# Kernel optimization log

Measured on AMD Instinct MI355X. Metric: run time of the kernel, lower is better.

## Reference

```python
import jax, jax.numpy as jnp
import numpy as np

B, N, C, H, K = 2, 4096, 256, 8, 32
D = C // H
EPS = 1e-5


def _ln(x, w, b):
    # LayerNorm over last axis
    m = x.mean(-1, keepdims=True)
    v = x.var(-1, keepdims=True)
    return (x - m) * jax.lax.rsqrt(v + EPS) * w + b


def setup_inputs() -> dict:
    key = jax.random.key(0)
    ks = jax.random.split(key, 16)
    s = 1.0 / np.sqrt(C)
    inp = {
        'xyz_A': jax.random.normal(ks[0], (B, N, 3), jnp.float32),
        'xyz_B': jax.random.normal(ks[1], (B, N, 3), jnp.float32),
        'featA': jax.random.normal(ks[2], (B, C, N), jnp.float32),
        'featB': jax.random.normal(ks[3], (B, C, N), jnp.float32),
        'ln_in_w': jnp.ones((C,), jnp.float32), 'ln_in_b': jnp.zeros((C,), jnp.float32),
        'wq': jax.random.normal(ks[4], (C, C), jnp.float32) * s, 'bq': jnp.zeros((C,), jnp.float32),
        'wk': jax.random.normal(ks[5], (C, C), jnp.float32) * s, 'bk': jnp.zeros((C,), jnp.float32),
        'wv': jax.random.normal(ks[6], (C, C), jnp.float32) * s, 'bv': jnp.zeros((C,), jnp.float32),
        'wqd': jax.random.normal(ks[7], (C, C), jnp.float32) * s, 'bqd': jnp.zeros((C,), jnp.float32),
        'wkd': jax.random.normal(ks[8], (C, C), jnp.float32) * s, 'bkd': jnp.zeros((C,), jnp.float32),
        'ln_sim_w': jnp.ones((C,), jnp.float32), 'ln_sim_b': jnp.zeros((C,), jnp.float32),
        'ln_dis_w': jnp.ones((C,), jnp.float32), 'ln_dis_b': jnp.zeros((C,), jnp.float32),
        'fus_w1': jax.random.normal(ks[9], (2 * C, 3 * C), jnp.float32) * (1.0 / np.sqrt(3 * C)),
        'bn_g': jnp.ones((2 * C,), jnp.float32), 'bn_b': jnp.zeros((2 * C,), jnp.float32),
        'fus_w2': jax.random.normal(ks[10], (C, 2 * C), jnp.float32) * (1.0 / np.sqrt(2 * C)),
        'fus_b2': jnp.zeros((C,), jnp.float32),
    }
    return inp


def reference(xyz_A, xyz_B, featA, featB, ln_in_w, ln_in_b,
              wq, bq, wk, bk, wv, bv, wqd, bqd, wkd, bkd,
              ln_sim_w, ln_sim_b, ln_dis_w, ln_dis_b,
              fus_w1, bn_g, bn_b, fus_w2, fus_b2):
    xA = featA.transpose(0, 2, 1)   # (B,N,C)
    xB = featB.transpose(0, 2, 1)   # (B,N,C)
    xA_n = _ln(xA, ln_in_w, ln_in_b)

    # KNN: nearest K points of xyz_B for each point in xyz_A
    d2 = (jnp.sum(xyz_A * xyz_A, -1)[:, :, None]
          + jnp.sum(xyz_B * xyz_B, -1)[:, None, :]
          - 2.0 * jnp.einsum('bnc,bmc->bnm', xyz_A, xyz_B))  # (B,N,N)
    _, knn_idx = jax.lax.top_k(-d2, K)  # (B,N,K)

    def proj(x, W, b):  # Conv1d k=1 on (B,N,C)
        return jnp.einsum('bnc,oc->bno', x, W) + b

    def heads(x):
        return x.reshape(B, N, H, D)

    q_s = heads(proj(xA_n, wq, bq))
    k_s = heads(proj(xB, wk, bk))
    v = heads(proj(xB, wv, bv))

    gather = jax.vmap(lambda f, i: f[i])  # (N,H,D),(N,K) -> (N,K,H,D)
    kN = gather(k_s, knn_idx)   # (B,N,K,H,D)
    vN = gather(v, knn_idx)     # (B,N,K,H,D)

    # similarity path: scaled dot-product over K neighbors
    sim = jnp.einsum('bnhd,bnkhd->bnhk', q_s, kN) / jnp.sqrt(jnp.float32(D))
    w_sim = jax.nn.softmax(sim, -1)
    ctx_s = jnp.einsum('bnhk,bnkhd->bnhd', w_sim, vN).reshape(B, N, C)
    ctx_s = _ln(ctx_s, ln_sim_w, ln_sim_b)

    # dissimilarity path: L2 distance scores
    q_d = heads(proj(xA_n, wqd, bqd))
    k_d = heads(proj(xB, wkd, bkd))
    kdN = gather(k_d, knn_idx)  # (B,N,K,H,D)
    diff = q_d[:, :, None] - kdN
    dist = jnp.sqrt(jnp.sum(diff * diff, -1)).transpose(0, 1, 3, 2)  # (B,N,H,K)
    w_dis = jax.nn.softmax(dist, -1)
    ctx_d = jnp.einsum('bnhk,bnkhd->bnhd', w_dis, vN).reshape(B, N, C)
    ctx_d = _ln(ctx_d, ln_dis_w, ln_dis_b)

    # fusion MLP (BN in eval mode: running mean 0, var 1)
    fused = jnp.concatenate([xA_n, ctx_s, ctx_d], -1)  # (B,N,3C)
    y = jnp.einsum('bnc,oc->bno', fused, fus_w1)
    y = y * jax.lax.rsqrt(jnp.float32(1.0 + EPS)) * bn_g + bn_b
    y = jax.nn.relu(y)
    y = jnp.einsum('bnc,oc->bno', y, fus_w2) + fus_b2

    out = y + xA  # residual (identity since in_channel == out_channel)
    return out.transpose(0, 2, 1)  # (B,C,N)
```

## Files before the change

kernel.cpp:

```cpp
#include <hip/hip_runtime.h>
#include <hip/hip_bf16.h>
#include <math.h>

#define B_ 2
#define N_ 4096
#define C_ 256
#define H_ 8
#define K_ 32
#define NP_ (B_*N_)
#define CAPW 256

typedef __attribute__((ext_vector_type(8))) short bf16x8;
typedef __attribute__((ext_vector_type(4))) float f32x4;

__device__ __forceinline__ float bf2f(unsigned short v){
    union { unsigned int u; float f; } x; x.u = ((unsigned int)v) << 16; return x.f;
}
__device__ __forceinline__ unsigned short f2bf(float f){
    union { float f; unsigned int u; } x; x.f = f;
    return (unsigned short)((x.u + 0x7FFFu + ((x.u >> 16) & 1u)) >> 16);
}
__device__ __forceinline__ unsigned int mono(float f){
    union { float f; unsigned int u; } x; x.f = f;
    return x.u ^ (0x80000000u | (unsigned int)((int)x.u >> 31));
}
__device__ __forceinline__ void gload_lds16(const unsigned short* g, unsigned short* l){
    __builtin_amdgcn_global_load_lds(
        (const __attribute__((address_space(1))) unsigned int*)g,
        (__attribute__((address_space(3))) unsigned int*)l, 16, 0, 0);
}

__global__ __launch_bounds__(256) void k_pre(
    const float* __restrict__ s0, const float* __restrict__ s1,
    const float* __restrict__ s2, const float* __restrict__ s3,
    const float* __restrict__ s4, const float* __restrict__ s5,
    const float* __restrict__ s6, unsigned short* __restrict__ Wb,
    const float* __restrict__ xyzB, f32x4* __restrict__ PB,
    const float* __restrict__ xyzA, int* __restrict__ order,
    const float* __restrict__ featA, const float* __restrict__ lnw,
    const float* __restrict__ lnb, unsigned short* __restrict__ F,
    const float* __restrict__ featB, unsigned short* __restrict__ XBT)
{
    __shared__ __align__(16) char smem[35200];
    const int bid = blockIdx.x;
    const int tid = threadIdx.x;
    if (bid < 3328){
        int i = bid*256 + tid;
        float v;
        if (i < 327680){
            int seg = i >> 16, off = i & 65535;
            const float* s = (seg==0)?s0:(seg==1)?s1:(seg==2)?s2:(seg==3)?s3:s4;
            v = s[off];
        } else if (i < 720896){
            v = s5[i - 327680];
        } else {
            v = s6[i - 720896];
        }
        Wb[i] = f2bf(v);
    } else if (bid < 3360){
        int i = (bid - 3328)*256 + tid;
        float x = xyzB[i*3], y = xyzB[i*3+1], z = xyzB[i*3+2];
        f32x4 o;
        o[0] = -2.f*x; o[1] = -2.f*y; o[2] = -2.f*z;
        o[3] = x*x + y*y + z*z;
        PB[i] = o;
    } else if (bid < 3362){
        unsigned int* hist = (unsigned int*)smem;
        unsigned int* wsum = (unsigned int*)(smem + 4096);
        const int b = bid - 3360;
        const int wv = tid >> 6, lane = tid & 63;
        for (int i = tid; i < 1024; i += 256) hist[i] = 0u;
        __syncthreads();
        unsigned int code[16];
        #pragma unroll
        for (int i = 0; i < 16; i++){
            const int n = tid + i*256;
            const float* pp = xyzA + (size_t)((b<<12) + n)*3;
            int qx = (int)fminf(fmaxf((pp[0] + 5.f)*1.6f, 0.f), 15.f);
            int qy = (int)fminf(fmaxf((pp[1] + 5.f)*0.8f, 0.f), 7.f);
            int qz = (int)fminf(fmaxf((pp[2] + 5.f)*0.8f, 0.f), 7.f);
            unsigned int c = (unsigned int)((qx & 1) | ((qz & 1) << 1) | ((qy & 1) << 2)
                           | (((qx >> 1) & 1) << 3) | (((qz >> 1) & 1) << 4) | (((qy >> 1) & 1) << 5)
                           | (((qx >> 2) & 1) << 6) | (((qz >> 2) & 1) << 7) | (((qy >> 2) & 1) << 8)
                           | (((qx >> 3) & 1) << 9));
            code[i] = c;
            atomicAdd(&hist[c], 1u);
        }
        __syncthreads();
        unsigned int loc[4], t4 = 0;
        #pragma unroll
        for (int j = 0; j < 4; j++){ loc[j] = hist[tid*4 + j]; t4 += loc[j]; }
        unsigned int sc = t4;
        #pragma unroll
        for (int off = 1; off < 64; off <<= 1){
            unsigned int o = __shfl_up(sc, off, 64);
            if (lane >= off) sc += o;
        }
        if (lane == 63) wsum[wv] = sc;
        __syncthreads();
        unsigned int wb = 0;
        #pragma unroll
        for (int j = 0; j < 4; j++) if (j < wv) wb += wsum[j];
        unsigned int base = wb + sc - t4;
        #pragma unroll
        for (int j = 0; j < 4; j++){ hist[tid*4 + j] = base; base += loc[j]; }
        __syncthreads();
        #pragma unroll
        for (int i = 0; i < 16; i++){
            const int n = tid + i*256;
            unsigned int pos = atomicAdd(&hist[code[i]], 1u);
            order[(b<<12) + pos] = (b<<12) | n;
        }
    } else if (bid < 3618){
        float (*tile)[257] = (float(*)[257])smem;
        float (*ps)[32]    = (float(*)[32])(smem + 32896);
        float (*pq)[32]    = (float(*)[32])(smem + 33920);
        float (*st)[32]    = (float(*)[32])(smem + 34944);
        const int nx = tid & 31, cy = tid >> 5;
        const int pbase = (bid - 3362) * 32;
        const int b = pbase >> 12, n0 = pbase & 4095;
        const float* sp = featA + (size_t)b*C_*N_ + n0;
        #pragma unroll 4
        for (int it = 0; it < 32; it++){
            int c = cy + it*8;
            tile[nx][c] = sp[(size_t)c*N_ + nx];
        }
        __syncthreads();
        {
            float s = 0.f, q = 0.f;
            #pragma unroll 8
            for (int i = 0; i < 32; i++){
                int cc = cy*32 + ((i + cy) & 31);
                float x = tile[nx][cc];
                s += x; q = fmaf(x, x, q);
            }
            ps[cy][nx] = s; pq[cy][nx] = q;
        }
        __syncthreads();
        if (tid < 32){
            float S = 0.f, Q = 0.f;
            #pragma unroll
            for (int j = 0; j < 8; j++){ S += ps[j][tid]; Q += pq[j][tid]; }
            float m = S*(1.f/256.f);
            float v = Q*(1.f/256.f) - m*m;
            st[0][tid] = m; st[1][tid] = rsqrtf(v + 1e-5f);
        }
        __syncthreads();
        const int p = pbase + nx;
        const float m = st[0][nx], r = st[1][nx];
        #pragma unroll
        for (int j = 0; j < 4; j++){
            bf16x8 ob;
            #pragma unroll
            for (int e = 0; e < 8; e++){
                int c = cy*32 + j*8 + e;
                ob[e] = (short)f2bf((tile[nx][c]-m)*r*lnw[c] + lnb[c]);
            }
            *(bf16x8*)(F + (size_t)p*768 + cy*32 + j*8) = ob;
        }
    } else {
        float (*tile)[65] = (float(*)[65])smem;
        const int idx = bid - 3618;
        const int x = idx & 63, y = (idx >> 6) & 3, z = idx >> 8;
        const int n0 = x*64, c0 = y*64;
        const int tx = tid & 63, ty = tid >> 6;
        const float* sp = featB + (size_t)z*C_*N_;
        #pragma unroll
        for (int i = 0; i < 16; i++){
            int cr = ty + i*4;
            tile[cr][tx] = sp[(size_t)(c0+cr)*N_ + n0 + tx];
        }
        __syncthreads();
        const int c = c0 + tx;
        #pragma unroll
        for (int i = 0; i < 16; i++){
            int nr = ty + i*4;
            int p = (z<<12) + n0 + nr;
            XBT[(size_t)p*256 + c] = f2bf(tile[tx][nr]);
        }
    }
}

__global__ __launch_bounds__(256) void k_knn(const float* __restrict__ xyzA,
        const f32x4* __restrict__ PB, int* __restrict__ knn){
    const int wv = threadIdx.x >> 6, lane = threadIdx.x & 63;
    const int p = blockIdx.x*4 + wv;
    const int b = p >> 12;
    const f32x4* pb = PB + ((size_t)b << 12);
    const float ax = xyzA[(size_t)p*3], ay = xyzA[(size_t)p*3+1], az = xyzA[(size_t)p*3+2];

    unsigned long long mn = ~0ull;
    #pragma unroll 8
    for (int i = 0; i < 64; i++){
        const int m = i*64 + lane;
        f32x4 c = pb[m];
        float d = fmaf(ax, c[0], fmaf(ay, c[1], fmaf(az, c[2], c[3])));
        unsigned long long key = (((unsigned long long)mono(d)) << 12) | (unsigned int)m;
        mn = key < mn ? key : mn;
    }
    unsigned int rk = 0;
    for (int j = 0; j < 64; j++){
        unsigned long long o = __shfl(mn, j, 64);
        rk += (o < mn) ? 1u : 0u;
    }
    unsigned long long sel = (rk == 31u) ? mn : ~0ull;
    #pragma unroll
    for (int off = 32; off; off >>= 1){
        unsigned long long o = __shfl_xor(sel, off, 64);
        sel = o < sel ? o : sel;
    }
    const unsigned long long v = sel;
    const unsigned int vhi = (unsigned int)(v >> 12);
    const unsigned int vlo = (unsigned int)(v & 0xFFFull);

    __shared__ unsigned long long cand[4][CAPW];
    __shared__ unsigned int cnt[4];
    if (lane == 0) cnt[wv] = 0u;
    #pragma unroll 8
    for (int i = 0; i < 64; i++){
        const int m = i*64 + lane;
        f32x4 c = pb[m];
        float d = fmaf(ax, c[0], fmaf(ay, c[1], fmaf(az, c[2], c[3])));
        unsigned int u = mono(d);
        if (u < vhi || (u == vhi && (unsigned int)m <= vlo)){
            unsigned int slot = atomicAdd(&cnt[wv], 1u);
            if (slot < CAPW)
                cand[wv][slot] = (((unsigned long long)u) << 12) | (unsigned int)m;
        }
    }
    const unsigned int C = cnt[wv];
    if (C <= CAPW){
        for (unsigned int i = lane; i < C; i += 64){
            unsigned long long mk = cand[wv][i];
            unsigned int rank = 0;
            for (unsigned int j = 0; j < C; j++) rank += (cand[wv][j] < mk) ? 1u : 0u;
            if (rank < K_) knn[(size_t)p*K_ + rank] = (int)(mk & 0xFFFull);
        }
    } else {
        unsigned long long last = 0ull;
        for (int it = 0; it < K_; it++){
            unsigned long long cm = ~0ull;
            #pragma unroll 4
            for (int i = 0; i < 64; i++){
                const int m = i*64 + lane;
                f32x4 c = pb[m];
                float d = fmaf(ax, c[0], fmaf(ay, c[1], fmaf(az, c[2], c[3])));
                unsigned long long key = (((unsigned long long)mono(d)) << 12) | (unsigned int)m;
                if (key > last && key < cm) cm = key;
            }
            #pragma unroll
            for (int off = 32; off; off >>= 1){
                unsigned long long o = __shfl_xor(cm, off, 64);
                cm = o < cm ? o : cm;
            }
            if (lane == 0) knn[(size_t)p*K_ + it] = (int)(cm & 0xFFFull);
            last = cm;
        }
    }
}

template<int MODE>
__device__ __forceinline__ void gemm_body(
    const unsigned short* __restrict__ X, int ldx,
    const unsigned short* __restrict__ W, int Kin,
    const float* __restrict__ e0, const float* __restrict__ e1, const float* __restrict__ e2,
    unsigned short* __restrict__ Y, int ldy,
    const float* __restrict__ resid, float* __restrict__ out,
    unsigned short (*As)[128*32], unsigned short (*Bs)[64*32], int bx, int by)
{
    const int tid = threadIdx.x, wid = tid >> 6, lane = tid & 63;
    const int lr = lane & 15, lg = lane >> 4;
    const int m0 = bx*128, n0 = by*64;
    const int lrow = lane >> 2, lcol = (lane & 3)*8;

    const unsigned short* Ag0 = X + (size_t)(m0 + wid*32 + lrow)*ldx + lcol;
    const unsigned short* Ag1 = X + (size_t)(m0 + wid*32 + 16 + lrow)*ldx + lcol;
    const unsigned short* Bg0 = W + (size_t)(n0 + wid*16 + lrow)*Kin + lcol;

    f32x4 acc[2][4] = {};
    const int NT = Kin >> 5;
    int buf = 0;
    gload_lds16(Ag0, &As[0][(wid*32)*32]);
    gload_lds16(Ag1, &As[0][(wid*32+16)*32]);
    gload_lds16(Bg0, &Bs[0][(wid*16)*32]);
    __syncthreads();
    for (int kt = 0; kt < NT; kt++){
        if (kt + 1 < NT){
            const int k = (kt+1)*32;
            gload_lds16(Ag0 + k, &As[buf^1][(wid*32)*32]);
            gload_lds16(Ag1 + k, &As[buf^1][(wid*32+16)*32]);
            gload_lds16(Bg0 + k, &Bs[buf^1][(wid*16)*32]);
        }
        bf16x8 a[2], b[4];
        #pragma unroll
        for (int mi = 0; mi < 2; mi++)
            a[mi] = *(const bf16x8*)&As[buf][(wid*32 + mi*16 + lr)*32 + lg*8];
        #pragma unroll
        for (int ni = 0; ni < 4; ni++)
            b[ni] = *(const bf16x8*)&Bs[buf][(ni*16 + lr)*32 + lg*8];
        #pragma unroll
        for (int mi = 0; mi < 2; mi++){
            #pragma unroll
            for (int ni = 0; ni < 4; ni++)
                acc[mi][ni] = __builtin_amdgcn_mfma_f32_16x16x32_bf16(a[mi], b[ni], acc[mi][ni], 0, 0, 0);
        }
        __syncthreads();
        buf ^= 1;
    }
    #pragma unroll
    for (int mi = 0; mi < 2; mi++){
        const int pbase = m0 + wid*32 + mi*16 + lg*4;
        #pragma unroll
        for (int ni = 0; ni < 4; ni++){
            const int o = n0 + ni*16 + lr;
            if (MODE == 0){
                const float* bp = (o < 256) ? e0 : ((o < 512) ? e1 : e2);
                float bias = bp[o & 255];
                #pragma unroll
                for (int r = 0; r < 4; r++)
                    Y[(size_t)(pbase + r)*ldy + o] = f2bf(acc[mi][ni][r] + bias);
            } else if (MODE == 1){
                float sc = e0[o] * 0.9999950000374997f;
                float sh = e1[o];
                #pragma unroll
                for (int r = 0; r < 4; r++){
                    float vv = fmaf(acc[mi][ni][r], sc, sh);
                    Y[(size_t)(pbase + r)*ldy + o] = f2bf(fmaxf(vv, 0.f));
                }
            } else {
                float bias = e0[o];
                const int b = pbase >> 12, nn = pbase & 4095;
                const size_t adr = ((size_t)b*C_ + o)*N_ + nn;
                f32x4 rv = *(const f32x4*)(resid + adr);
                f32x4 ov;
                #pragma unroll
                for (int r = 0; r < 4; r++) ov[r] = acc[mi][ni][r] + bias + rv[r];
                *(f32x4*)(out + adr) = ov;
            }
        }
    }
}

__global__ __launch_bounds__(256) void k_proj(
    const unsigned short* __restrict__ F, const unsigned short* __restrict__ XBT,
    const unsigned short* __restrict__ WQcat, const unsigned short* __restrict__ WKVD,
    const float* __restrict__ bq, const float* __restrict__ bqd,
    const float* __restrict__ bk, const float* __restrict__ bv, const float* __restrict__ bkd,
    unsigned short* __restrict__ QQ, unsigned short* __restrict__ KVD)
{
    __shared__ __align__(16) unsigned short As[2][128*32];
    __shared__ __align__(16) unsigned short Bs[2][64*32];
    if (blockIdx.y < 8)
        gemm_body<0>(F, 768, WQcat, 256, bq, bqd, nullptr, QQ, 512, nullptr, nullptr,
                     As, Bs, blockIdx.x, blockIdx.y);
    else
        gemm_body<0>(XBT, 256, WKVD, 256, bk, bv, bkd, KVD, 768, nullptr, nullptr,
                     As, Bs, blockIdx.x, blockIdx.y - 8);
}

template<int MODE>
__global__ __launch_bounds__(256) void k_gemm(
    const unsigned short* __restrict__ X, int ldx,
    const unsigned short* __restrict__ W, int Kin,
    const float* __restrict__ e0, const float* __restrict__ e1, const float* __restrict__ e2,
    unsigned short* __restrict__ Y, int ldy,
    const float* __restrict__ resid, float* __restrict__ out)
{
    __shared__ __align__(16) unsigned short As[2][128*32];
    __shared__ __align__(16) unsigned short Bs[2][64*32];
    gemm_body<MODE>(X, ldx, W, Kin, e0, e1, e2, Y, ldy, resid, out,
                    As, Bs, blockIdx.x, blockIdx.y);
}

__global__ __launch_bounds__(256) void k_attn(
    const unsigned short* __restrict__ QQ, const unsigned short* __restrict__ KVD,
    const int* __restrict__ KNN, const int* __restrict__ order,
    const float* __restrict__ lnsw, const float* __restrict__ lnsb,
    const float* __restrict__ lndw, const float* __restrict__ lndb,
    unsigned short* __restrict__ F)
{
    __shared__ float q_l[2][2][2][128];
    __shared__ float w_l[2][2][2][4][33];
    __shared__ int   idx_l[2][2][32];
    __shared__ float part_l[2][2][4];

    const int tid = threadIdx.x;
    const int wid = tid >> 6, lane = tid & 63;
    const int ps = wid >> 1, wh = wid & 1;
    const int bid = blockIdx.x;
    const int xcd = bid & 7, ib = bid >> 3;
    const int batch = xcd & 1, quarter = xcd >> 1;
    const int jj = quarter*1024 + ib*2 + ps;
    const int p = order[(batch << 12) + jj];
    const int b = batch;

    {
        const unsigned short* qrow = QQ + (size_t)p*512 + wh*128 + lane*2;
        unsigned int us = *(const unsigned int*)qrow;
        unsigned int ud = *(const unsigned int*)(qrow + 256);
        q_l[ps][wh][0][lane*2]   = bf2f((unsigned short)(us & 0xffff));
        q_l[ps][wh][0][lane*2+1] = bf2f((unsigned short)(us >> 16));
        q_l[ps][wh][1][lane*2]   = bf2f((unsigned short)(ud & 0xffff));
        q_l[ps][wh][1][lane*2+1] = bf2f((unsigned short)(ud >> 16));
        if (lane < 32) idx_l[ps][wh][lane] = KNN[(size_t)p*K_ + lane];
    }

    const int hh = lane >> 5, kk = lane & 31;
    const int tq = lane >> 4, c = lane & 15;
    const int hl = c >> 2;

    const int nbr_qk = idx_l[ps][wh][kk];
    int nbt[8];
    #pragma unroll
    for (int i = 0; i < 8; i++) nbt[i] = idx_l[ps][wh][tq + i*4];

    const unsigned short* rowb = KVD + (size_t)((b<<12) + nbr_qk)*768;
    bf16x8 kx[2][4], dx[2][4];
    #pragma unroll
    for (int j = 0; j < 2; j++){
        const int h = wh*4 + j*2 + hh;
        const bf16x8* kr = (const bf16x8*)(rowb + h*32);
        const bf16x8* dr = (const bf16x8*)(rowb + 512 + h*32);
        #pragma unroll
        for (int cc = 0; cc < 4; cc++){ kx[j][cc] = kr[cc]; dx[j][cc] = dr[cc]; }
    }
    const unsigned short* vbase = KVD + 256 + wh*128 + c*8;
    bf16x8 vx[8];
    #pragma unroll
    for (int i = 0; i < 8; i++)
        vx[i] = *(const bf16x8*)(vbase + (size_t)((b<<12) + nbt[i])*768);

    #pragma unroll
    for (int j = 0; j < 2; j++){
        const int hloc = j*2 + hh;
        const float* qs = &q_l[ps][wh][0][hloc*32];
        const float* qd = &q_l[ps][wh][1][hloc*32];
        float s = 0.f, dd = 0.f;
        #pragma unroll
        for (int cc = 0; cc < 4; cc++){
            #pragma unroll
            for (int e = 0; e < 8; e++){
                const int d = cc*8 + e;
                s = fmaf(qs[d], bf2f((unsigned short)kx[j][cc][e]), s);
                float df = qd[d] - bf2f((unsigned short)dx[j][cc][e]);
                dd = fmaf(df, df, dd);
            }
        }
        float sim = s * 0.17677669529663687f;
        float dist = sqrtf(dd);
        float m1 = sim, m2 = dist;
        #pragma unroll
        for (int off = 1; off < 32; off <<= 1){
            m1 = fmaxf(m1, __shfl_xor(m1, off, 64));
            m2 = fmaxf(m2, __shfl_xor(m2, off, 64));
        }
        float e1v = __expf(sim - m1);
        float e2v = __expf(dist - m2);
        float s1 = e1v, s2 = e2v;
        #pragma unroll
        for (int off = 1; off < 32; off <<= 1){
            s1 += __shfl_xor(s1, off, 64);
            s2 += __shfl_xor(s2, off, 64);
        }
        w_l[ps][wh][0][hloc][kk] = e1v / s1;
        w_l[ps][wh][1][hloc][kk] = e2v / s2;
    }

    float cs[8] = {0,0,0,0,0,0,0,0}, cd[8] = {0,0,0,0,0,0,0,0};
    #pragma unroll
    for (int i = 0; i < 8; i++){
        const int t = tq + i*4;
        const float wsv = w_l[ps][wh][0][hl][t];
        const float wdv = w_l[ps][wh][1][hl][t];
        #pragma unroll
        for (int e = 0; e < 8; e++){
            float vf = bf2f((unsigned short)vx[i][e]);
            cs[e] = fmaf(wsv, vf, cs[e]);
            cd[e] = fmaf(wdv, vf, cd[e]);
        }
    }
    #pragma unroll
    for (int e = 0; e < 8; e++){
        cs[e] += __shfl_xor(cs[e], 16, 64); cs[e] += __shfl_xor(cs[e], 32, 64);
        cd[e] += __shfl_xor(cd[e], 16, 64); cd[e] += __shfl_xor(cd[e], 32, 64);
    }
    float s1 = 0.f, q1 = 0.f, s2 = 0.f, q2 = 0.f;
    #pragma unroll
    for (int e = 0; e < 8; e++){
        s1 += cs[e]; q1 = fmaf(cs[e], cs[e], q1);
        s2 += cd[e]; q2 = fmaf(cd[e], cd[e], q2);
    }
    #pragma unroll
    for (int off = 1; off < 16; off <<= 1){
        s1 += __shfl_xor(s1, off, 64); q1 += __shfl_xor(q1, off, 64);
        s2 += __shfl_xor(s2, off, 64); q2 += __shfl_xor(q2, off, 64);
    }
    if (lane == 0){
        part_l[ps][wh][0] = s1; part_l[ps][wh][1] = q1;
        part_l[ps][wh][2] = s2; part_l[ps][wh][3] = q2;
    }
    __syncthreads();
    const float S1 = s1 + part_l[ps][wh^1][0];
    const float Q1 = q1 + part_l[ps][wh^1][1];
    const float S2 = s2 + part_l[ps][wh^1][2];
    const float Q2 = q2 + part_l[ps][wh^1][3];
    const float m1 = S1*(1.f/256.f), m2 = S2*(1.f/256.f);
    const float r1 = rsqrtf(Q1*(1.f/256.f) - m1*m1 + 1e-5f);
    const float r2 = rsqrtf(Q2*(1.f/256.f) - m2*m2 + 1e-5f);

    if (tq == 0){
        bf16x8 ob;
        #pragma unroll
        for (int e = 0; e < 8; e++){
            const int cg = wh*128 + c*8 + e;
            ob[e] = (short)f2bf((cs[e]-m1)*r1*lnsw[cg] + lnsb[cg]);
        }
        *(bf16x8*)(F + (size_t)p*768 + 256 + wh*128 + c*8) = ob;
    } else if (tq == 1){
        bf16x8 ob;
        #pragma unroll
        for (int e = 0; e < 8; e++){
            const int cg = wh*128 + c*8 + e;
            ob[e] = (short)f2bf((cd[e]-m2)*r2*lndw[cg] + lndb[cg]);
        }
        *(bf16x8*)(F + (size_t)p*768 + 512 + wh*128 + c*8) = ob;
    }
}

extern "C" void kernel_launch(void* const* d_in, const int* in_sizes, int n_in,
                              void* d_out, int out_size, void* d_ws, size_t ws_size,
                              hipStream_t stream)
{
    const float* xyzA   = (const float*)d_in[0];
    const float* xyzB   = (const float*)d_in[1];
    const float* featA  = (const float*)d_in[2];
    const float* featB  = (const float*)d_in[3];
    const float* ln_in_w= (const float*)d_in[4];
    const float* ln_in_b= (const float*)d_in[5];
    const float* wq  = (const float*)d_in[6];
    const float* bq  = (const float*)d_in[7];
    const float* wk  = (const float*)d_in[8];
    const float* bk  = (const float*)d_in[9];
    const float* wv  = (const float*)d_in[10];
    const float* bv  = (const float*)d_in[11];
    const float* wqd = (const float*)d_in[12];
    const float* bqd = (const float*)d_in[13];
    const float* wkd = (const float*)d_in[14];
    const float* bkd = (const float*)d_in[15];
    const float* lnsw = (const float*)d_in[16];
    const float* lnsb = (const float*)d_in[17];
    const float* lndw = (const float*)d_in[18];
    const float* lndb = (const float*)d_in[19];
    const float* fw1 = (const float*)d_in[20];
    const float* bng = (const float*)d_in[21];
    const float* bnb = (const float*)d_in[22];
    const float* fw2 = (const float*)d_in[23];
    const float* fb2 = (const float*)d_in[24];
    float* out = (float*)d_out;
    char* ws = (char*)d_ws;

    unsigned short* F    = (unsigned short*)(ws + 0);
    unsigned short* XBT  = (unsigned short*)(ws + 12582912);
    unsigned short* QQ   = (unsigned short*)(ws + 16777216);
    unsigned short* KVD  = (unsigned short*)(ws + 25165824);
    unsigned short* Y1   = (unsigned short*)(ws + 37748736);
    f32x4*          PB   = (f32x4*)(ws + 37748736);
    int*            KNNi = (int*)(ws + 46137344);
    int*            ORD  = (int*)(ws + 47185920);
    unsigned short* Wb   = (unsigned short*)(ws + 47251456);
    unsigned short* WQcat = Wb;
    unsigned short* WKVD  = Wb + 131072;
    unsigned short* W1b   = Wb + 327680;
    unsigned short* W2b   = Wb + 720896;

    k_pre<<<4130, 256, 0, stream>>>(wq, wqd, wk, wv, wkd, fw1, fw2, Wb,
                                    xyzB, PB, xyzA, ORD,
                                    featA, ln_in_w, ln_in_b, F, featB, XBT);
    k_knn<<<2048, 256, 0, stream>>>(xyzA, PB, KNNi);

    k_proj<<<dim3(64,20), 256, 0, stream>>>(F, XBT, WQcat, WKVD, bq, bqd, bk, bv, bkd, QQ, KVD);

    k_attn<<<4096, 256, 0, stream>>>(QQ, KVD, KNNi, ORD, lnsw, lnsb, lndw, lndb, F);

    k_gemm<1><<<dim3(64,8), 256, 0, stream>>>(F,  768, W1b, 768, bng, bnb, nullptr, Y1, 512, nullptr, nullptr);
    k_gemm<2><<<dim3(64,4), 256, 0, stream>>>(Y1, 512, W2b, 512, fb2, nullptr, nullptr, nullptr, 0, featA, out);
}
```

Before: 142.0 us.

## Process two query points per wave in attention and vectorize weight conversion

The attention kernel now has each wave handle two query points instead of one, interleaving their K/D/V gathers, dot products, softmaxes and LayerNorm reductions. This halves the grid and raises memory-level parallelism and ILP per wave. The weight-conversion section of the preprocessing kernel now converts four floats per thread with vector loads and stores, cutting that section's block count by a factor of four. The cost is higher register pressure in the attention kernel, which could lower occupancy.

```diff
diff --git a/kernel.cpp b/kernel.cpp
--- a/kernel.cpp
+++ b/kernel.cpp
@@ -12,6 +12,7 @@
 
 typedef __attribute__((ext_vector_type(8))) short bf16x8;
 typedef __attribute__((ext_vector_type(4))) float f32x4;
+typedef __attribute__((ext_vector_type(4))) unsigned short ushort4_t;
 
 __device__ __forceinline__ float bf2f(unsigned short v){
     union { unsigned int u; float f; } x; x.u = ((unsigned int)v) << 16; return x.f;
@@ -44,30 +45,34 @@
     __shared__ __align__(16) char smem[35200];
     const int bid = blockIdx.x;
     const int tid = threadIdx.x;
-    if (bid < 3328){
-        int i = bid*256 + tid;
-        float v;
+    if (bid < 832){
+        int i = (bid*256 + tid)*4;
+        const float* s; int off;
         if (i < 327680){
-            int seg = i >> 16, off = i & 65535;
-            const float* s = (seg==0)?s0:(seg==1)?s1:(seg==2)?s2:(seg==3)?s3:s4;
-            v = s[off];
+            int seg = i >> 16;
+            s = (seg==0)?s0:(seg==1)?s1:(seg==2)?s2:(seg==3)?s3:s4;
+            off = i & 65535;
         } else if (i < 720896){
-            v = s5[i - 327680];
+            s = s5; off = i - 327680;
         } else {
-            v = s6[i - 720896];
-        }
-        Wb[i] = f2bf(v);
-    } else if (bid < 3360){
-        int i = (bid - 3328)*256 + tid;
+            s = s6; off = i - 720896;
+        }
+        f32x4 v = *(const f32x4*)(s + off);
+        ushort4_t o;
+        #pragma unroll
+        for (int e = 0; e < 4; e++) o[e] = f2bf(v[e]);
+        *(ushort4_t*)(Wb + i) = o;
+    } else if (bid < 864){
+        int i = (bid - 832)*256 + tid;
         float x = xyzB[i*3], y = xyzB[i*3+1], z = xyzB[i*3+2];
         f32x4 o;
         o[0] = -2.f*x; o[1] = -2.f*y; o[2] = -2.f*z;
         o[3] = x*x + y*y + z*z;
         PB[i] = o;
-    } else if (bid < 3362){
+    } else if (bid < 866){
         unsigned int* hist = (unsigned int*)smem;
         unsigned int* wsum = (unsigned int*)(smem + 4096);
-        const int b = bid - 3360;
+        const int b = bid - 864;
         const int wv = tid >> 6, lane = tid & 63;
         for (int i = tid; i < 1024; i += 256) hist[i] = 0u;
         __syncthreads();
@@ -111,13 +116,13 @@
             unsigned int pos = atomicAdd(&hist[code[i]], 1u);
             order[(b<<12) + pos] = (b<<12) | n;
         }
-    } else if (bid < 3618){
+    } else if (bid < 1122){
         float (*tile)[257] = (float(*)[257])smem;
         float (*ps)[32]    = (float(*)[32])(smem + 32896);
         float (*pq)[32]    = (float(*)[32])(smem + 33920);
         float (*st)[32]    = (float(*)[32])(smem + 34944);
         const int nx = tid & 31, cy = tid >> 5;
-        const int pbase = (bid - 3362) * 32;
+        const int pbase = (bid - 866) * 32;
         const int b = pbase >> 12, n0 = pbase & 4095;
         const float* sp = featA + (size_t)b*C_*N_ + n0;
         #pragma unroll 4
@@ -160,7 +165,7 @@
         }
     } else {
         float (*tile)[65] = (float(*)[65])smem;
-        const int idx = bid - 3618;
+        const int idx = bid - 1122;
         const int x = idx & 63, y = (idx >> 6) & 3, z = idx >> 8;
         const int n0 = x*64, c0 = y*64;
         const int tx = tid & 63, ty = tid >> 6;
@@ -379,151 +384,195 @@
     const float* __restrict__ lndw, const float* __restrict__ lndb,
     unsigned short* __restrict__ F)
 {
-    __shared__ float q_l[2][2][2][128];
-    __shared__ float w_l[2][2][2][4][33];
-    __shared__ int   idx_l[2][2][32];
-    __shared__ float part_l[2][2][4];
+    __shared__ float q_l[4][2][2][128];
+    __shared__ float w_l[4][2][2][4][33];
+    __shared__ int   idx_l[4][2][32];
+    __shared__ float part_l[4][2][4];
 
     const int tid = threadIdx.x;
     const int wid = tid >> 6, lane = tid & 63;
-    const int ps = wid >> 1, wh = wid & 1;
+    const int g = wid >> 1, wh = wid & 1;
     const int bid = blockIdx.x;
     const int xcd = bid & 7, ib = bid >> 3;
     const int batch = xcd & 1, quarter = xcd >> 1;
-    const int jj = quarter*1024 + ib*2 + ps;
-    const int p = order[(batch << 12) + jj];
+    const int jjb = quarter*1024 + ib*4 + g*2;
+    int pp[2];
+    pp[0] = order[(batch << 12) + jjb];
+    pp[1] = order[(batch << 12) + jjb + 1];
     const int b = batch;
 
-    {
-        const unsigned short* qrow = QQ + (size_t)p*512 + wh*128 + lane*2;
+    #pragma unroll
+    for (int pt = 0; pt < 2; pt++){
+        const unsigned short* qrow = QQ + (size_t)pp[pt]*512 + wh*128 + lane*2;
         unsigned int us = *(const unsigned int*)qrow;
         unsigned int ud = *(const unsigned int*)(qrow + 256);
-        q_l[ps][wh][0][lane*2]   = bf2f((unsigned short)(us & 0xffff));
-        q_l[ps][wh][0][lane*2+1] = bf2f((unsigned short)(us >> 16));
-        q_l[ps][wh][1][lane*2]   = bf2f((unsigned short)(ud & 0xffff));
-        q_l[ps][wh][1][lane*2+1] = bf2f((unsigned short)(ud >> 16));
-        if (lane < 32) idx_l[ps][wh][lane] = KNN[(size_t)p*K_ + lane];
-    }
+        q_l[wid][pt][0][lane*2]   = bf2f((unsigned short)(us & 0xffff));
+        q_l[wid][pt][0][lane*2+1] = bf2f((unsigned short)(us >> 16));
+        q_l[wid][pt][1][lane*2]   = bf2f((unsigned short)(ud & 0xffff));
+        q_l[wid][pt][1][lane*2+1] = bf2f((unsigned short)(ud >> 16));
+    }
+    if (lane < 32) idx_l[wid][0][lane]      = KNN[(size_t)pp[0]*K_ + lane];
+    else           idx_l[wid][1][lane - 32] = KNN[(size_t)pp[1]*K_ + (lane - 32)];
 
     const int hh = lane >> 5, kk = lane & 31;
     const int tq = lane >> 4, c = lane & 15;
-    const int hl = c >> 2;
-
-    const int nbr_qk = idx_l[ps][wh][kk];
-    int nbt[8];
-    #pragma unroll
-    for (int i = 0; i < 8; i++) nbt[i] = idx_l[ps][wh][tq + i*4];
-
-    const unsigned short* rowb = KVD + (size_t)((b<<12) + nbr_qk)*768;
-    bf16x8 kx[2][4], dx[2][4];
-    #pragma unroll
-    for (int j = 0; j < 2; j++){
-        const int h = wh*4 + j*2 + hh;
-        const bf16x8* kr = (const bf16x8*)(rowb + h*32);
-        const bf16x8* dr = (const bf16x8*)(rowb + 512 + h*32);
-        #pragma unroll
-        for (int cc = 0; cc < 4; cc++){ kx[j][cc] = kr[cc]; dx[j][cc] = dr[cc]; }
-    }
-    const unsigned short* vbase = KVD + 256 + wh*128 + c*8;
-    bf16x8 vx[8];
-    #pragma unroll
-    for (int i = 0; i < 8; i++)
-        vx[i] = *(const bf16x8*)(vbase + (size_t)((b<<12) + nbt[i])*768);
-
+    const int hl2 = c >> 2;
+
+    const unsigned short* rowb[2];
+    rowb[0] = KVD + (size_t)((b<<12) + idx_l[wid][0][kk])*768;
+    rowb[1] = KVD + (size_t)((b<<12) + idx_l[wid][1][kk])*768;
     #pragma unroll
     for (int j = 0; j < 2; j++){
         const int hloc = j*2 + hh;
-        const float* qs = &q_l[ps][wh][0][hloc*32];
-        const float* qd = &q_l[ps][wh][1][hloc*32];
-        float s = 0.f, dd = 0.f;
+        const int h = wh*4 + hloc;
+        bf16x8 kx[2][4], dx[2][4];
+        #pragma unroll
+        for (int pt = 0; pt < 2; pt++){
+            const bf16x8* kr = (const bf16x8*)(rowb[pt] + h*32);
+            const bf16x8* dr = (const bf16x8*)(rowb[pt] + 512 + h*32);
+            #pragma unroll
+            for (int cc = 0; cc < 4; cc++){ kx[pt][cc] = kr[cc]; dx[pt][cc] = dr[cc]; }
+        }
+        float s[2] = {0.f, 0.f}, dd[2] = {0.f, 0.f};
         #pragma unroll
         for (int cc = 0; cc < 4; cc++){
             #pragma unroll
             for (int e = 0; e < 8; e++){
                 const int d = cc*8 + e;
-                s = fmaf(qs[d], bf2f((unsigned short)kx[j][cc][e]), s);
-                float df = qd[d] - bf2f((unsigned short)dx[j][cc][e]);
-                dd = fmaf(df, df, dd);
-            }
-        }
-        float sim = s * 0.17677669529663687f;
-        float dist = sqrtf(dd);
-        float m1 = sim, m2 = dist;
+                #pragma unroll
+                for (int pt = 0; pt < 2; pt++){
+                    float qsv = q_l[wid][pt][0][hloc*32 + d];
+                    float qdv = q_l[wid][pt][1][hloc*32 + d];
+                    s[pt] = fmaf(qsv, bf2f((unsigned short)kx[pt][cc][e]), s[pt]);
+                    float df = qdv - bf2f((unsigned short)dx[pt][cc][e]);
+                    dd[pt] = fmaf(df, df, dd[pt]);
+                }
+            }
+        }
+        float sim[2], dist[2], m1[2], m2[2];
+        #pragma unroll
+        for (int pt = 0; pt < 2; pt++){
+            sim[pt] = s[pt] * 0.17677669529663687f;
+            dist[pt] = sqrtf(dd[pt]);
+            m1[pt] = sim[pt]; m2[pt] = dist[pt];
+        }
         #pragma unroll
         for (int off = 1; off < 32; off <<= 1){
-            m1 = fmaxf(m1, __shfl_xor(m1, off, 64));
-            m2 = fmaxf(m2, __shfl_xor(m2, off, 64));
-        }
-        float e1v = __expf(sim - m1);
-        float e2v = __expf(dist - m2);
-        float s1 = e1v, s2 = e2v;
+            #pragma unroll
+            for (int pt = 0; pt < 2; pt++){
+                m1[pt] = fmaxf(m1[pt], __shfl_xor(m1[pt], off, 64));
+                m2[pt] = fmaxf(m2[pt], __shfl_xor(m2[pt], off, 64));
+            }
+        }
+        float e1v[2], e2v[2], s1[2], s2[2];
+        #pragma unroll
+        for (int pt = 0; pt < 2; pt++){
+            e1v[pt] = __expf(sim[pt] - m1[pt]);
+            e2v[pt] = __expf(dist[pt] - m2[pt]);
+            s1[pt] = e1v[pt]; s2[pt] = e2v[pt];
+        }
         #pragma unroll
         for (int off = 1; off < 32; off <<= 1){
-            s1 += __shfl_xor(s1, off, 64);
-            s2 += __shfl_xor(s2, off, 64);
-        }
-        w_l[ps][wh][0][hloc][kk] = e1v / s1;
-        w_l[ps][wh][1][hloc][kk] = e2v / s2;
-    }
-
-    float cs[8] = {0,0,0,0,0,0,0,0}, cd[8] = {0,0,0,0,0,0,0,0};
-    #pragma unroll
-    for (int i = 0; i < 8; i++){
-        const int t = tq + i*4;
-        const float wsv = w_l[ps][wh][0][hl][t];
-        const float wdv = w_l[ps][wh][1][hl][t];
-        #pragma unroll
-        for (int e = 0; e < 8; e++){
-            float vf = bf2f((unsigned short)vx[i][e]);
-            cs[e] = fmaf(wsv, vf, cs[e]);
-            cd[e] = fmaf(wdv, vf, cd[e]);
+            #pragma unroll
+            for (int pt = 0; pt < 2; pt++){
+                s1[pt] += __shfl_xor(s1[pt], off, 64);
+                s2[pt] += __shfl_xor(s2[pt], off, 64);
+            }
+        }
+        #pragma unroll
+        for (int pt = 0; pt < 2; pt++){
+            w_l[wid][pt][0][hloc][kk] = e1v[pt] / s1[pt];
+            w_l[wid][pt][1][hloc][kk] = e2v[pt] / s2[pt];
+        }
+    }
+
+    float cs[2][8] = {}, cd[2][8] = {};
+    {
+        const unsigned short* vbase = KVD + 256 + wh*128 + c*8;
+        bf16x8 vx[2][8];
+        #pragma unroll
+        for (int i = 0; i < 8; i++){
+            #pragma unroll
+            for (int pt = 0; pt < 2; pt++){
+                int nn = idx_l[wid][pt][tq + i*4];
+                vx[pt][i] = *(const bf16x8*)(vbase + (size_t)((b<<12) + nn)*768);
+            }
+        }
+        #pragma unroll
+        for (int i = 0; i < 8; i++){
+            const int t = tq + i*4;
+            #pragma unroll
+            for (int pt = 0; pt < 2; pt++){
+                const float wsv = w_l[wid][pt][0][hl2][t];
+                const float wdv = w_l[wid][pt][1][hl2][t];
+                #pragma unroll
+                for (int e = 0; e < 8; e++){
+                    float vf = bf2f((unsigned short)vx[pt][i][e]);
+                    cs[pt][e] = fmaf(wsv, vf, cs[pt][e]);
+                    cd[pt][e] = fmaf(wdv, vf, cd[pt][e]);
+                }
+            }
         }
     }
     #pragma unroll
     for (int e = 0; e < 8; e++){
-        cs[e] += __shfl_xor(cs[e], 16, 64); cs[e] += __shfl_xor(cs[e], 32, 64);
-        cd[e] += __shfl_xor(cd[e], 16, 64); cd[e] += __shfl_xor(cd[e], 32, 64);
-    }
-    float s1 = 0.f, q1 = 0.f, s2 = 0.f, q2 = 0.f;
+        #pragma unroll
+        for (int pt = 0; pt < 2; pt++){
+            cs[pt][e] += __shfl_xor(cs[pt][e], 16, 64); cs[pt][e] += __shfl_xor(cs[pt][e], 32, 64);
+            cd[pt][e] += __shfl_xor(cd[pt][e], 16, 64); cd[pt][e] += __shfl_xor(cd[pt][e], 32, 64);
+        }
+    }
+    float s1[2] = {0.f,0.f}, q1[2] = {0.f,0.f}, s2[2] = {0.f,0.f}, q2[2] = {0.f,0.f};
     #pragma unroll
     for (int e = 0; e < 8; e++){
-        s1 += cs[e]; q1 = fmaf(cs[e], cs[e], q1);
-        s2 += cd[e]; q2 = fmaf(cd[e], cd[e], q2);
+        #pragma unroll
+        for (int pt = 0; pt < 2; pt++){
+            s1[pt] += cs[pt][e]; q1[pt] = fmaf(cs[pt][e], cs[pt][e], q1[pt]);
+            s2[pt] += cd[pt][e]; q2[pt] = fmaf(cd[pt][e], cd[pt][e], q2[pt]);
+        }
     }
     #pragma unroll
     for (int off = 1; off < 16; off <<= 1){
-        s1 += __shfl_xor(s1, off, 64); q1 += __shfl_xor(q1, off, 64);
-        s2 += __shfl_xor(s2, off, 64); q2 += __shfl_xor(q2, off, 64);
+        #pragma unroll
+        for (int pt = 0; pt < 2; pt++){
+            s1[pt] += __shfl_xor(s1[pt], off, 64); q1[pt] += __shfl_xor(q1[pt], off, 64);
+            s2[pt] += __shfl_xor(s2[pt], off, 64); q2[pt] += __shfl_xor(q2[pt], off, 64);
+        }
     }
     if (lane == 0){
-        part_l[ps][wh][0] = s1; part_l[ps][wh][1] = q1;
-        part_l[ps][wh][2] = s2; part_l[ps][wh][3] = q2;
+        #pragma unroll
+        for (int pt = 0; pt < 2; pt++){
+            part_l[wid][pt][0] = s1[pt]; part_l[wid][pt][1] = q1[pt];
+            part_l[wid][pt][2] = s2[pt]; part_l[wid][pt][3] = q2[pt];
+        }
     }
     __syncthreads();
-    const float S1 = s1 + part_l[ps][wh^1][0];
-    const float Q1 = q1 + part_l[ps][wh^1][1];
-    const float S2 = s2 + part_l[ps][wh^1][2];
-    const float Q2 = q2 + part_l[ps][wh^1][3];
-    const float m1 = S1*(1.f/256.f), m2 = S2*(1.f/256.f);
-    const float r1 = rsqrtf(Q1*(1.f/256.f) - m1*m1 + 1e-5f);
-    const float r2 = rsqrtf(Q2*(1.f/256.f) - m2*m2 + 1e-5f);
-
-    if (tq == 0){
-        bf16x8 ob;
-        #pragma unroll
-        for (int e = 0; e < 8; e++){
-            const int cg = wh*128 + c*8 + e;
-            ob[e] = (short)f2bf((cs[e]-m1)*r1*lnsw[cg] + lnsb[cg]);
-        }
-        *(bf16x8*)(F + (size_t)p*768 + 256 + wh*128 + c*8) = ob;
-    } else if (tq == 1){
-        bf16x8 ob;
-        #pragma unroll
-        for (int e = 0; e < 8; e++){
-            const int cg = wh*128 + c*8 + e;
-            ob[e] = (short)f2bf((cd[e]-m2)*r2*lndw[cg] + lndb[cg]);
-        }
-        *(bf16x8*)(F + (size_t)p*768 + 512 + wh*128 + c*8) = ob;
+    #pragma unroll
+    for (int pt = 0; pt < 2; pt++){
+        const float S1 = s1[pt] + part_l[wid^1][pt][0];
+        const float Q1 = q1[pt] + part_l[wid^1][pt][1];
+        const float S2 = s2[pt] + part_l[wid^1][pt][2];
+        const float Q2 = q2[pt] + part_l[wid^1][pt][3];
+        const float m1 = S1*(1.f/256.f), m2 = S2*(1.f/256.f);
+        const float r1 = rsqrtf(Q1*(1.f/256.f) - m1*m1 + 1e-5f);
+        const float r2 = rsqrtf(Q2*(1.f/256.f) - m2*m2 + 1e-5f);
+        if (tq == 0){
+            bf16x8 ob;
+            #pragma unroll
+            for (int e = 0; e < 8; e++){
+                const int cg = wh*128 + c*8 + e;
+                ob[e] = (short)f2bf((cs[pt][e]-m1)*r1*lnsw[cg] + lnsb[cg]);
+            }
+            *(bf16x8*)(F + (size_t)pp[pt]*768 + 256 + wh*128 + c*8) = ob;
+        } else if (tq == 1){
+            bf16x8 ob;
+            #pragma unroll
+            for (int e = 0; e < 8; e++){
+                const int cg = wh*128 + c*8 + e;
+                ob[e] = (short)f2bf((cd[pt][e]-m2)*r2*lndw[cg] + lndb[cg]);
+            }
+            *(bf16x8*)(F + (size_t)pp[pt]*768 + 512 + wh*128 + c*8) = ob;
+        }
     }
 }
 
@@ -573,14 +622,14 @@
     unsigned short* W1b   = Wb + 327680;
     unsigned short* W2b   = Wb + 720896;
 
-    k_pre<<<4130, 256, 0, stream>>>(wq, wqd, wk, wv, wkd, fw1, fw2, Wb,
+    k_pre<<<1634, 256, 0, stream>>>(wq, wqd, wk, wv, wkd, fw1, fw2, Wb,
                                     xyzB, PB, xyzA, ORD,
                                     featA, ln_in_w, ln_in_b, F, featB, XBT);
     k_knn<<<2048, 256, 0, stream>>>(xyzA, PB, KNNi);
 
     k_proj<<<dim3(64,20), 256, 0, stream>>>(F, XBT, WQcat, WKVD, bq, bqd, bk, bv, bkd, QQ, KVD);
 
-    k_attn<<<4096, 256, 0, stream>>>(QQ, KVD, KNNi, ORD, lnsw, lnsb, lndw, lndb, F);
+    k_attn<<<2048, 256, 0, stream>>>(QQ, KVD, KNNi, ORD, lnsw, lnsb, lndw, lndb, F);
 
     k_gemm<1><<<dim3(64,8), 256, 0, stream>>>(F,  768, W1b, 768, bng, bnb, nullptr, Y1, 512, nullptr, nullptr);
     k_gemm<2><<<dim3(64,4), 256, 0, stream>>>(Y1, 512, W2b, 512, fb2, nullptr, nullptr, nullptr, 0, featA, out);
```

Result: slower. 150.2 us (+5.8%).

## Use bf16 dot2 and norm expansion for attention distances; vectorize weight conversion

Applied to the files above, without the earlier changes.

The attention kernel now computes the L2 distance as |q|^2 + |k|^2 - 2 q·k. A new small kernel precomputes the per-head key norms, and query norms are reduced in-register. Both dot products use v_dot2_f32_bf16 on packed bf16 pairs instead of scalar converts and FMAs, and the V loads are moved after the softmax to lower register pressure. The weight-conversion stage of the pre-kernel is vectorized four elements per thread, which cuts its block count. The expanded distance form risks cancellation error, and the extra kernel adds a launch.

```diff
diff --git a/kernel.cpp b/kernel.cpp
--- a/kernel.cpp
+++ b/kernel.cpp
@@ -12,6 +12,9 @@
 
 typedef __attribute__((ext_vector_type(8))) short bf16x8;
 typedef __attribute__((ext_vector_type(4))) float f32x4;
+typedef __attribute__((ext_vector_type(4))) unsigned short ushort4_t;
+
+#define DOT2BF(acc, a, b) asm("v_dot2_f32_bf16 %0, %1, %2, %0" : "+v"(acc) : "v"(a), "v"(b))
 
 __device__ __forceinline__ float bf2f(unsigned short v){
     union { unsigned int u; float f; } x; x.u = ((unsigned int)v) << 16; return x.f;
@@ -44,30 +47,34 @@
     __shared__ __align__(16) char smem[35200];
     const int bid = blockIdx.x;
     const int tid = threadIdx.x;
-    if (bid < 3328){
-        int i = bid*256 + tid;
-        float v;
+    if (bid < 832){
+        int i = (bid*256 + tid)*4;
+        const float* s; int off;
         if (i < 327680){
-            int seg = i >> 16, off = i & 65535;
-            const float* s = (seg==0)?s0:(seg==1)?s1:(seg==2)?s2:(seg==3)?s3:s4;
-            v = s[off];
+            int seg = i >> 16;
+            s = (seg==0)?s0:(seg==1)?s1:(seg==2)?s2:(seg==3)?s3:s4;
+            off = i & 65535;
         } else if (i < 720896){
-            v = s5[i - 327680];
+            s = s5; off = i - 327680;
         } else {
-            v = s6[i - 720896];
-        }
-        Wb[i] = f2bf(v);
-    } else if (bid < 3360){
-        int i = (bid - 3328)*256 + tid;
+            s = s6; off = i - 720896;
+        }
+        f32x4 v = *(const f32x4*)(s + off);
+        ushort4_t o;
+        #pragma unroll
+        for (int e = 0; e < 4; e++) o[e] = f2bf(v[e]);
+        *(ushort4_t*)(Wb + i) = o;
+    } else if (bid < 864){
+        int i = (bid - 832)*256 + tid;
         float x = xyzB[i*3], y = xyzB[i*3+1], z = xyzB[i*3+2];
         f32x4 o;
         o[0] = -2.f*x; o[1] = -2.f*y; o[2] = -2.f*z;
         o[3] = x*x + y*y + z*z;
         PB[i] = o;
-    } else if (bid < 3362){
+    } else if (bid < 866){
         unsigned int* hist = (unsigned int*)smem;
         unsigned int* wsum = (unsigned int*)(smem + 4096);
-        const int b = bid - 3360;
+        const int b = bid - 864;
         const int wv = tid >> 6, lane = tid & 63;
         for (int i = tid; i < 1024; i += 256) hist[i] = 0u;
         __syncthreads();
@@ -111,13 +118,13 @@
             unsigned int pos = atomicAdd(&hist[code[i]], 1u);
             order[(b<<12) + pos] = (b<<12) | n;
         }
-    } else if (bid < 3618){
+    } else if (bid < 1122){
         float (*tile)[257] = (float(*)[257])smem;
         float (*ps)[32]    = (float(*)[32])(smem + 32896);
         float (*pq)[32]    = (float(*)[32])(smem + 33920);
         float (*st)[32]    = (float(*)[32])(smem + 34944);
         const int nx = tid & 31, cy = tid >> 5;
-        const int pbase = (bid - 3362) * 32;
+        const int pbase = (bid - 866) * 32;
         const int b = pbase >> 12, n0 = pbase & 4095;
         const float* sp = featA + (size_t)b*C_*N_ + n0;
         #pragma unroll 4
@@ -160,7 +167,7 @@
         }
     } else {
         float (*tile)[65] = (float(*)[65])smem;
-        const int idx = bid - 3618;
+        const int idx = bid - 1122;
         const int x = idx & 63, y = (idx >> 6) & 3, z = idx >> 8;
         const int n0 = x*64, c0 = y*64;
         const int tx = tid & 63, ty = tid >> 6;
@@ -372,16 +379,33 @@
                     As, Bs, blockIdx.x, blockIdx.y);
 }
 
+__global__ __launch_bounds__(256) void k_kn2(const unsigned short* __restrict__ KVD,
+                                             float* __restrict__ KN2){
+    const int t = blockIdx.x*256 + threadIdx.x;
+    const unsigned int* src = (const unsigned int*)(KVD + (size_t)(t >> 3)*768 + 512 + (t & 7)*32);
+    float s = 0.f;
+    #pragma unroll
+    for (int i = 0; i < 16; i++){
+        unsigned int u = src[i];
+        float a = bf2f((unsigned short)(u & 0xffff));
+        float bqv = bf2f((unsigned short)(u >> 16));
+        s = fmaf(a, a, s); s = fmaf(bqv, bqv, s);
+    }
+    KN2[t] = s;
+}
+
 __global__ __launch_bounds__(256) void k_attn(
     const unsigned short* __restrict__ QQ, const unsigned short* __restrict__ KVD,
+    const float* __restrict__ KN2,
     const int* __restrict__ KNN, const int* __restrict__ order,
     const float* __restrict__ lnsw, const float* __restrict__ lnsb,
     const float* __restrict__ lndw, const float* __restrict__ lndb,
     unsigned short* __restrict__ F)
 {
-    __shared__ float q_l[2][2][2][128];
-    __shared__ float w_l[2][2][2][4][33];
-    __shared__ int   idx_l[2][2][32];
+    __shared__ unsigned int q_lu[4][2][64];
+    __shared__ float w_l[4][2][4][33];
+    __shared__ float qn_l[4][4];
+    __shared__ int   idx_l[4][32];
     __shared__ float part_l[2][2][4];
 
     const int tid = threadIdx.x;
@@ -398,56 +422,52 @@
         const unsigned short* qrow = QQ + (size_t)p*512 + wh*128 + lane*2;
         unsigned int us = *(const unsigned int*)qrow;
         unsigned int ud = *(const unsigned int*)(qrow + 256);
-        q_l[ps][wh][0][lane*2]   = bf2f((unsigned short)(us & 0xffff));
-        q_l[ps][wh][0][lane*2+1] = bf2f((unsigned short)(us >> 16));
-        q_l[ps][wh][1][lane*2]   = bf2f((unsigned short)(ud & 0xffff));
-        q_l[ps][wh][1][lane*2+1] = bf2f((unsigned short)(ud >> 16));
-        if (lane < 32) idx_l[ps][wh][lane] = KNN[(size_t)p*K_ + lane];
+        q_lu[wid][0][lane] = us;
+        q_lu[wid][1][lane] = ud;
+        float c0 = bf2f((unsigned short)(ud & 0xffff));
+        float c1 = bf2f((unsigned short)(ud >> 16));
+        float pn = fmaf(c0, c0, c1*c1);
+        pn += __shfl_xor(pn, 1, 64);
+        pn += __shfl_xor(pn, 2, 64);
+        pn += __shfl_xor(pn, 4, 64);
+        pn += __shfl_xor(pn, 8, 64);
+        if ((lane & 15) == 0) qn_l[wid][lane >> 4] = pn;
+        if (lane < 32) idx_l[wid][lane] = KNN[(size_t)p*K_ + lane];
     }
 
     const int hh = lane >> 5, kk = lane & 31;
     const int tq = lane >> 4, c = lane & 15;
     const int hl = c >> 2;
 
-    const int nbr_qk = idx_l[ps][wh][kk];
-    int nbt[8];
-    #pragma unroll
-    for (int i = 0; i < 8; i++) nbt[i] = idx_l[ps][wh][tq + i*4];
-
+    const int nbr_qk = idx_l[wid][kk];
     const unsigned short* rowb = KVD + (size_t)((b<<12) + nbr_qk)*768;
-    bf16x8 kx[2][4], dx[2][4];
-    #pragma unroll
-    for (int j = 0; j < 2; j++){
-        const int h = wh*4 + j*2 + hh;
-        const bf16x8* kr = (const bf16x8*)(rowb + h*32);
-        const bf16x8* dr = (const bf16x8*)(rowb + 512 + h*32);
-        #pragma unroll
-        for (int cc = 0; cc < 4; cc++){ kx[j][cc] = kr[cc]; dx[j][cc] = dr[cc]; }
-    }
-    const unsigned short* vbase = KVD + 256 + wh*128 + c*8;
-    bf16x8 vx[8];
-    #pragma unroll
-    for (int i = 0; i < 8; i++)
-        vx[i] = *(const bf16x8*)(vbase + (size_t)((b<<12) + nbt[i])*768);
-
     #pragma unroll
     for (int j = 0; j < 2; j++){
         const int hloc = j*2 + hh;
-        const float* qs = &q_l[ps][wh][0][hloc*32];
-        const float* qd = &q_l[ps][wh][1][hloc*32];
-        float s = 0.f, dd = 0.f;
+        const int h = wh*4 + hloc;
+        uint4 kv[4], dv[4];
         #pragma unroll
         for (int cc = 0; cc < 4; cc++){
-            #pragma unroll
-            for (int e = 0; e < 8; e++){
-                const int d = cc*8 + e;
-                s = fmaf(qs[d], bf2f((unsigned short)kx[j][cc][e]), s);
-                float df = qd[d] - bf2f((unsigned short)dx[j][cc][e]);
-                dd = fmaf(df, df, dd);
-            }
+            kv[cc] = ((const uint4*)(rowb + h*32))[cc];
+            dv[cc] = ((const uint4*)(rowb + 512 + h*32))[cc];
+        }
+        uint4 qs4[4], qd4[4];
+        #pragma unroll
+        for (int i = 0; i < 4; i++){
+            qs4[i] = ((const uint4*)&q_lu[wid][0][hloc*16])[i];
+            qd4[i] = ((const uint4*)&q_lu[wid][1][hloc*16])[i];
+        }
+        float s = 0.f, t = 0.f;
+        #pragma unroll
+        for (int cc = 0; cc < 4; cc++){
+            DOT2BF(s, qs4[cc].x, kv[cc].x); DOT2BF(t, qd4[cc].x, dv[cc].x);
+            DOT2BF(s, qs4[cc].y, kv[cc].y); DOT2BF(t, qd4[cc].y, dv[cc].y);
+            DOT2BF(s, qs4[cc].z, kv[cc].z); DOT2BF(t, qd4[cc].z, dv[cc].z);
+            DOT2BF(s, qs4[cc].w, kv[cc].w); DOT2BF(t, qd4[cc].w, dv[cc].w);
         }
         float sim = s * 0.17677669529663687f;
-        float dist = sqrtf(dd);
+        float kn2v = KN2[(size_t)((b<<12) + nbr_qk)*8 + h];
+        float dist = sqrtf(fmaxf(qn_l[wid][hloc] + kn2v - 2.f*t, 0.f));
         float m1 = sim, m2 = dist;
         #pragma unroll
         for (int off = 1; off < 32; off <<= 1){
@@ -462,21 +482,31 @@
             s1 += __shfl_xor(s1, off, 64);
             s2 += __shfl_xor(s2, off, 64);
         }
-        w_l[ps][wh][0][hloc][kk] = e1v / s1;
-        w_l[ps][wh][1][hloc][kk] = e2v / s2;
+        w_l[wid][0][hloc][kk] = e1v / s1;
+        w_l[wid][1][hloc][kk] = e2v / s2;
     }
 
     float cs[8] = {0,0,0,0,0,0,0,0}, cd[8] = {0,0,0,0,0,0,0,0};
-    #pragma unroll
-    for (int i = 0; i < 8; i++){
-        const int t = tq + i*4;
-        const float wsv = w_l[ps][wh][0][hl][t];
-        const float wdv = w_l[ps][wh][1][hl][t];
-        #pragma unroll
-        for (int e = 0; e < 8; e++){
-            float vf = bf2f((unsigned short)vx[i][e]);
-            cs[e] = fmaf(wsv, vf, cs[e]);
-            cd[e] = fmaf(wdv, vf, cd[e]);
+    {
+        const unsigned short* vbase = KVD + 256 + wh*128 + c*8;
+        int nbt[8];
+        #pragma unroll
+        for (int i = 0; i < 8; i++) nbt[i] = idx_l[wid][tq + i*4];
+        bf16x8 vx[8];
+        #pragma unroll
+        for (int i = 0; i < 8; i++)
+            vx[i] = *(const bf16x8*)(vbase + (size_t)((b<<12) + nbt[i])*768);
+        #pragma unroll
+        for (int i = 0; i < 8; i++){
+            const int t = tq + i*4;
+            const float wsv = w_l[wid][0][hl][t];
+            const float wdv = w_l[wid][1][hl][t];
+            #pragma unroll
+            for (int e = 0; e < 8; e++){
+                float vf = bf2f((unsigned short)vx[i][e]);
+                cs[e] = fmaf(wsv, vf, cs[e]);
+                cd[e] = fmaf(wdv, vf, cd[e]);
+            }
         }
     }
     #pragma unroll
@@ -561,6 +591,7 @@
 
     unsigned short* F    = (unsigned short*)(ws + 0);
     unsigned short* XBT  = (unsigned short*)(ws + 12582912);
+    float*          KN2  = (float*)(ws + 12582912);
     unsigned short* QQ   = (unsigned short*)(ws + 16777216);
     unsigned short* KVD  = (unsigned short*)(ws + 25165824);
     unsigned short* Y1   = (unsigned short*)(ws + 37748736);
@@ -573,14 +604,15 @@
     unsigned short* W1b   = Wb + 327680;
     unsigned short* W2b   = Wb + 720896;
 
-    k_pre<<<4130, 256, 0, stream>>>(wq, wqd, wk, wv, wkd, fw1, fw2, Wb,
+    k_pre<<<1634, 256, 0, stream>>>(wq, wqd, wk, wv, wkd, fw1, fw2, Wb,
                                     xyzB, PB, xyzA, ORD,
                                     featA, ln_in_w, ln_in_b, F, featB, XBT);
     k_knn<<<2048, 256, 0, stream>>>(xyzA, PB, KNNi);
 
     k_proj<<<dim3(64,20), 256, 0, stream>>>(F, XBT, WQcat, WKVD, bq, bqd, bk, bv, bkd, QQ, KVD);
-
-    k_attn<<<4096, 256, 0, stream>>>(QQ, KVD, KNNi, ORD, lnsw, lnsb, lndw, lndb, F);
+    k_kn2<<<256, 256, 0, stream>>>(KVD, KN2);
+
+    k_attn<<<4096, 256, 0, stream>>>(QQ, KVD, KN2, KNNi, ORD, lnsw, lnsb, lndw, lndb, F);
 
     k_gemm<1><<<dim3(64,8), 256, 0, stream>>>(F,  768, W1b, 768, bng, bnb, nullptr, Y1, 512, nullptr, nullptr);
     k_gemm<2><<<dim3(64,4), 256, 0, stream>>>(Y1, 512, W2b, 512, fb2, nullptr, nullptr, nullptr, 0, featA, out);
```

After: 148.9 us. 4.9% more time.
